# Performance work log

Hardware: AMD Instinct MI355X
Metric: run time of the kernel (lower is better)

## Reference

```python
import jax, jax.numpy as jnp
import numpy as np

B, S, D = 4, 4096, 128

def setup_inputs() -> dict:
    key = jax.random.key(0)
    kq, kk, kv = jax.random.split(key, 3)
    q = jax.random.normal(kq, (B, S, D), dtype=jnp.float32)
    k = jax.random.normal(kk, (B, S, D), dtype=jnp.float32)
    v = jax.random.normal(kv, (B, S, D), dtype=jnp.float32)
    return {"q": q, "k": k, "v": v}

def reference(q, k, v):
    d_model = q.shape[-1]
    scale = 1.0 / jnp.sqrt(jnp.asarray(d_model, q.dtype))
    # [B, S, S] scores
    scores = jnp.einsum('bqd,bkd->bqk', q, k) * scale
    s = q.shape[1]
    causal = jnp.tril(jnp.ones((s, s), dtype=bool))
    neg_inf = jnp.asarray(-jnp.inf, scores.dtype)
    scores = jnp.where(causal[None, :, :], scores, neg_inf)
    attn = jax.nn.softmax(scores, axis=-1)
    return jnp.einsum('bqk,bkd->bqd', attn, v)
```

## Files before the change

### kernel.cpp

```cpp
#include <hip/hip_runtime.h>


#define B_   4
#define S_   4096
#define D_   128
#define BM   64
#define BN   64
#define NT_  (S_ / BM)
#define RMAX 4
#define PSTR 72
#define BLOB_SHORTS 16384

typedef __attribute__((ext_vector_type(8))) short bf16x8;
typedef __attribute__((ext_vector_type(4))) float f32x4;

__device__ __forceinline__ short f2bf(float x) {
    unsigned u = __builtin_bit_cast(unsigned, x);
    unsigned r = (u + 0x7fffu + ((u >> 16) & 1u)) >> 16;
    return (short)r;
}
__device__ __forceinline__ float ex2(float x) { return __builtin_amdgcn_exp2f(x); }

__device__ __forceinline__ void gl_lds16(const short* g, short* l) {
    __builtin_amdgcn_global_load_lds(
        (const __attribute__((address_space(1))) unsigned int*)g,
        (__attribute__((address_space(3))) unsigned int*)l, 16, 0, 0);
}

__global__ __launch_bounds__(256) void prep(const float* __restrict__ Qg,
                                            const float* __restrict__ Kg,
                                            const float* __restrict__ Vg,
                                            short* __restrict__ Qbf,
                                            short* __restrict__ KV)
{
    __shared__ short vt[64][136];

    const int x = blockIdx.x;
    const int b = x & 3, tile = x >> 2;
    const int tid = threadIdx.x;
    const int n = tid >> 2, q = tid & 3;
    const size_t rowbase = ((size_t)b * S_ + (size_t)tile * 64 + n) * D_ + q * 32;
    short* blob = KV + (size_t)(b * NT_ + tile) * BLOB_SHORTS;

    const float SC = 0.12751740f;
    {
        const float4* src = reinterpret_cast<const float4*>(Qg + rowbase);
        short* dst = Qbf + rowbase;
#pragma unroll
        for (int j = 0; j < 4; ++j) {
            float4 a = src[2 * j], c = src[2 * j + 1];
            bf16x8 v;
            v[0] = f2bf(a.x * SC); v[1] = f2bf(a.y * SC); v[2] = f2bf(a.z * SC); v[3] = f2bf(a.w * SC);
            v[4] = f2bf(c.x * SC); v[5] = f2bf(c.y * SC); v[6] = f2bf(c.z * SC); v[7] = f2bf(c.w * SC);
            *reinterpret_cast<bf16x8*>(dst + j * 8) = v;
        }
    }
    {
        const float4* src = reinterpret_cast<const float4*>(Kg + rowbase);
#pragma unroll
        for (int j = 0; j < 4; ++j) {
            float4 a = src[2 * j], c = src[2 * j + 1];
            bf16x8 v;
            v[0] = f2bf(a.x); v[1] = f2bf(a.y); v[2] = f2bf(a.z); v[3] = f2bf(a.w);
            v[4] = f2bf(c.x); v[5] = f2bf(c.y); v[6] = f2bf(c.z); v[7] = f2bf(c.w);
            const int G = q * 4 + j;
            const int p = (G & 8) | ((G & 7) ^ (n & 7));
            *reinterpret_cast<bf16x8*>(blob + n * 128 + p * 8) = v;
        }
    }
    {
        const float4* src = reinterpret_cast<const float4*>(Vg + rowbase);
#pragma unroll
        for (int j = 0; j < 4; ++j) {
            float4 a = src[2 * j], c = src[2 * j + 1];
            bf16x8 v;
            v[0] = f2bf(a.x); v[1] = f2bf(a.y); v[2] = f2bf(a.z); v[3] = f2bf(a.w);
            v[4] = f2bf(c.x); v[5] = f2bf(c.y); v[6] = f2bf(c.z); v[7] = f2bf(c.w);
            *reinterpret_cast<bf16x8*>(&vt[n][q * 32 + j * 8]) = v;
        }
    }
    __syncthreads();
    {
        const int d = tid >> 1, jj = tid & 1;
#pragma unroll
        for (int j = 0; j < 4; ++j) {
            const int G = jj * 4 + j;
            bf16x8 g;
#pragma unroll
            for (int i = 0; i < 8; ++i) g[i] = vt[G * 8 + i][d];
            const int p = G ^ (d & 7);
            *reinterpret_cast<bf16x8*>(blob + 8192 + d * 64 + p * 8) = g;
        }
    }
}

template<bool SPLIT>
__global__ __launch_bounds__(256) void fa_fwd(const short* __restrict__ Qbf,
                                              const short* __restrict__ KV,
                                              float* __restrict__ Og,
                                              float* __restrict__ Op,
                                              float* __restrict__ Ml,
                                              int R)
{
    __shared__ short lkv[2][BLOB_SHORTS];
    __shared__ short lp[4 * 16 * PSTR];

    const int tid  = threadIdx.x;
    const int wv   = tid >> 6;
    const int lane = tid & 63;
    const int m    = lane & 15;
    const int quad = lane >> 4;
    const int m7   = m & 7;

    int batch, t, lo, hi, chunk_id;
    {
        const int id = blockIdx.x;
        batch = id & 3;
        if (SPLIT) {
            int u = id >> 2;
            int tt = u / R;
            int r  = u - tt * R;
            t  = NT_ - 1 - tt;
            lo = r * (t + 1) / R;
            hi = (r + 1) * (t + 1) / R;
            chunk_id = (batch * NT_ + t) * R + r;
            if (lo >= hi) return;
        } else {
            t  = NT_ - 1 - (id >> 2);
            lo = 0; hi = t + 1; chunk_id = 0;
        }
    }

    bf16x8 qf[4];
    {
        const short* qp = Qbf + ((size_t)batch * S_ + (size_t)t * BM + wv * 16 + m) * D_ + quad * 8;
#pragma unroll
        for (int c = 0; c < 4; ++c)
            qf[c] = *reinterpret_cast<const bf16x8*>(qp + c * 32);
    }

    f32x4 acc[8];
#pragma unroll
    for (int i = 0; i < 8; ++i) acc[i] = (f32x4){0.f, 0.f, 0.f, 0.f};
    float mrun[4], lrun[4];
#pragma unroll
    for (int r = 0; r < 4; ++r) { mrun[r] = -__builtin_inff(); lrun[r] = 0.f; }

    short* pw = lp + wv * 16 * PSTR;

    const size_t tilebase = (size_t)batch * NT_ * BLOB_SHORTS;
#define STAGE(KT, BUF) do {                                                   \
        const short* g_ = KV + tilebase + (size_t)(KT) * BLOB_SHORTS          \
                          + wv * 4096 + lane * 8;                             \
        short* l_ = (BUF) + wv * 4096;                                        \
        _Pragma("unroll")                                                     \
        for (int c_ = 0; c_ < 8; ++c_)                                        \
            gl_lds16(g_ + c_ * 512, l_ + c_ * 512);                           \
    } while (0)

    STAGE(lo, lkv[0]);

    for (int kt = lo; kt < hi; ++kt) {
        short* cur = lkv[(kt - lo) & 1];
        short* nxt = lkv[(kt - lo + 1) & 1];
        __syncthreads();
        if (kt + 1 < hi) STAGE(kt + 1, nxt);

        const short* lk = cur;
        const short* lv = cur + 8192;

        f32x4 s[4];
#pragma unroll
        for (int nt = 0; nt < 4; ++nt) s[nt] = (f32x4){0.f, 0.f, 0.f, 0.f};
#pragma unroll
        for (int c = 0; c < 4; ++c) {
            const int p = ((c >> 1) * 8) | ((((c & 1) * 4) | quad) ^ m7);
#pragma unroll
            for (int nt = 0; nt < 4; ++nt) {
                bf16x8 kf = *reinterpret_cast<const bf16x8*>(lk + nt * 2048 + m * 128 + p * 8);
                s[nt] = __builtin_amdgcn_mfma_f32_16x16x32_bf16(qf[c], kf, s[nt], 0, 0, 0);
            }
        }

        if (kt == t) {
            const int qloc = wv * 16 + quad * 4;
#pragma unroll
            for (int nt = 0; nt < 4; ++nt) {
                const int kloc = nt * 16 + m;
#pragma unroll
                for (int r = 0; r < 4; ++r)
                    if (kloc > qloc + r) s[nt][r] = -__builtin_inff();
            }
        }

#pragma unroll
        for (int r = 0; r < 4; ++r) {
            float mx = fmaxf(fmaxf(s[0][r], s[1][r]), fmaxf(s[2][r], s[3][r]));
#pragma unroll
            for (int off = 1; off < 16; off <<= 1) mx = fmaxf(mx, __shfl_xor(mx, off));
            float mnew = fmaxf(mrun[r], mx);
            float al   = ex2(mrun[r] - mnew);
            mrun[r] = mnew;
            float p0 = ex2(s[0][r] - mnew);
            float p1 = ex2(s[1][r] - mnew);
            float p2 = ex2(s[2][r] - mnew);
            float p3 = ex2(s[3][r] - mnew);
            s[0][r] = p0; s[1][r] = p1; s[2][r] = p2; s[3][r] = p3;
            float sum = (p0 + p1) + (p2 + p3);
#pragma unroll
            for (int off = 1; off < 16; off <<= 1) sum += __shfl_xor(sum, off);
            lrun[r] = lrun[r] * al + sum;
#pragma unroll
            for (int ct = 0; ct < 8; ++ct) acc[ct][r] *= al;
        }

#pragma unroll
        for (int nt = 0; nt < 4; ++nt)
#pragma unroll
            for (int r = 0; r < 4; ++r)
                pw[(quad * 4 + r) * PSTR + nt * 16 + m] = f2bf(s[nt][r]);

#pragma unroll
        for (int ks = 0; ks < 2; ++ks) {
            bf16x8 pf = *reinterpret_cast<const bf16x8*>(pw + m * PSTR + ks * 32 + quad * 8);
            const int p = (ks * 4 + quad) ^ m7;
#pragma unroll
            for (int ct = 0; ct < 8; ++ct) {
                bf16x8 vf = *reinterpret_cast<const bf16x8*>(lv + ct * 1024 + m * 64 + p * 8);
                acc[ct] = __builtin_amdgcn_mfma_f32_16x16x32_bf16(pf, vf, acc[ct], 0, 0, 0);
            }
        }
    }
#undef STAGE

    const int row0 = wv * 16 + quad * 4;
    if (SPLIT) {
        float* ob = Op + (size_t)chunk_id * (BM * D_);
#pragma unroll
        for (int r = 0; r < 4; ++r)
#pragma unroll
            for (int ct = 0; ct < 8; ++ct)
                ob[(row0 + r) * D_ + ct * 16 + m] = acc[ct][r];
        if (m == 0) {
            float* mlb = Ml + (size_t)chunk_id * (BM * 2);
#pragma unroll
            for (int r = 0; r < 4; ++r) {
                mlb[(row0 + r) * 2]     = mrun[r];
                mlb[(row0 + r) * 2 + 1] = lrun[r];
            }
        }
    } else {
        const size_t obase = ((size_t)batch * S_ + (size_t)t * BM + row0) * D_;
#pragma unroll
        for (int r = 0; r < 4; ++r) {
            float inv = 1.0f / lrun[r];
#pragma unroll
            for (int ct = 0; ct < 8; ++ct)
                Og[obase + (size_t)r * D_ + ct * 16 + m] = acc[ct][r] * inv;
        }
    }
}

template<int RR>
__global__ __launch_bounds__(256) void fa_merge(const float* __restrict__ Op,
                                                const float* __restrict__ Ml,
                                                float* __restrict__ Og)
{
    const int x   = blockIdx.x;
    const int btq = x >> 2;
    const int seg = x & 3;
    const int t   = btq & (NT_ - 1);
    const int row = seg * 16 + (threadIdx.x >> 4);
    const int cg  = threadIdx.x & 15;
    const size_t cbase = (size_t)btq * RR;

    float mg = -__builtin_inff();
#pragma unroll
    for (int r = 0; r < RR; ++r) {
        int lo = r * (t + 1) / RR, hi = (r + 1) * (t + 1) / RR;
        if (lo < hi) mg = fmaxf(mg, Ml[(cbase + r) * (BM * 2) + row * 2]);
    }
    float l = 0.f;
    f32x4 a0 = (f32x4){0.f, 0.f, 0.f, 0.f}, a1 = a0;
#pragma unroll
    for (int r = 0; r < RR; ++r) {
        int lo = r * (t + 1) / RR, hi = (r + 1) * (t + 1) / RR;
        if (lo >= hi) continue;
        float mr = Ml[(cbase + r) * (BM * 2) + row * 2];
        float lr = Ml[(cbase + r) * (BM * 2) + row * 2 + 1];
        float w  = ex2(mr - mg);
        l += lr * w;
        const f32x4* op = reinterpret_cast<const f32x4*>(Op + (cbase + r) * (BM * D_) + row * D_ + cg * 8);
        a0 += w * op[0]; a1 += w * op[1];
    }
    float inv = 1.0f / l;
    f32x4* og = reinterpret_cast<f32x4*>(Og + (size_t)btq * (BM * D_) + row * D_ + cg * 8);
    og[0] = a0 * inv; og[1] = a1 * inv;
}

extern "C" void kernel_launch(void* const* d_in, const int* in_sizes, int n_in,
                              void* d_out, int out_size, void* d_ws, size_t ws_size,
                              hipStream_t stream) {
    const float* q = (const float*)d_in[0];
    const float* k = (const float*)d_in[1];
    const float* v = (const float*)d_in[2];
    float* o = (float*)d_out;

    const size_t QBF_BYTES = (size_t)B_ * S_ * D_ * 2;
    const size_t KV_BYTES  = (size_t)B_ * NT_ * BLOB_SHORTS * 2;
    const size_t PREFIX    = QBF_BYTES + KV_BYTES;
    const size_t O_FLOATS  = (size_t)B_ * NT_ * BM * D_;
    const size_t ML_FLOATS = (size_t)B_ * NT_ * BM * 2;
    const size_t PER_R     = (O_FLOATS + ML_FLOATS) * sizeof(float);

    char* ws = (char*)d_ws;
    short* Qbf = (short*)ws;
    short* KV  = (short*)(ws + QBF_BYTES);

    int R = 0;
    if (ws_size > PREFIX) {
        R = (int)((ws_size - PREFIX) / PER_R);
        if (R > RMAX) R = RMAX;
    }

    prep<<<dim3(B_ * NT_), 256, 0, stream>>>(q, k, v, Qbf, KV);

    if (R >= 1) {
        float* Op = (float*)(ws + PREFIX);
        float* Ml = Op + (size_t)R * O_FLOATS;
        fa_fwd<true><<<dim3(B_ * NT_ * R), 256, 0, stream>>>(Qbf, KV, nullptr, Op, Ml, R);
        switch (R) {
            case 1: fa_merge<1><<<dim3(B_ * NT_ * 4), 256, 0, stream>>>(Op, Ml, o); break;
            case 2: fa_merge<2><<<dim3(B_ * NT_ * 4), 256, 0, stream>>>(Op, Ml, o); break;
            case 3: fa_merge<3><<<dim3(B_ * NT_ * 4), 256, 0, stream>>>(Op, Ml, o); break;
            default: fa_merge<4><<<dim3(B_ * NT_ * 4), 256, 0, stream>>>(Op, Ml, o); break;
        }
    } else {
        fa_fwd<false><<<dim3(B_ * NT_), 256, 0, stream>>>(Qbf, KV, o, nullptr, nullptr, 1);
    }
}
```

Before: 134.9 us.

## Transpose QK MFMA, shuffle P in registers, single LDS buffer, finer prep/merge grids

New measurement: 195.4 us. +44.9%, slower.

```diff
diff --git a/kernel.cpp b/kernel.cpp
--- a/kernel.cpp
+++ b/kernel.cpp
@@ -8,7 +8,6 @@
 #define BN   64
 #define NT_  (S_ / BM)
 #define RMAX 4
-#define PSTR 72
 #define BLOB_SHORTS 16384
 
 typedef __attribute__((ext_vector_type(8))) short bf16x8;
@@ -20,11 +19,8 @@
     return (short)r;
 }
 __device__ __forceinline__ float ex2(float x) { return __builtin_amdgcn_exp2f(x); }
-
-__device__ __forceinline__ void gl_lds16(const short* g, short* l) {
-    __builtin_amdgcn_global_load_lds(
-        (const __attribute__((address_space(1))) unsigned int*)g,
-        (__attribute__((address_space(3))) unsigned int*)l, 16, 0, 0);
+__device__ __forceinline__ unsigned pkbf(float lo, float hi) {
+    return (unsigned)(unsigned short)f2bf(lo) | ((unsigned)(unsigned short)f2bf(hi) << 16);
 }
 
 __global__ __launch_bounds__(256) void prep(const float* __restrict__ Qg,
@@ -33,61 +29,55 @@
                                             short* __restrict__ Qbf,
                                             short* __restrict__ KV)
 {
-    __shared__ short vt[64][136];
-
-    const int x = blockIdx.x;
-    const int b = x & 3, tile = x >> 2;
+    __shared__ short vt[64][40];
+    const int id  = blockIdx.x;
     const int tid = threadIdx.x;
-    const int n = tid >> 2, q = tid & 3;
-    const size_t rowbase = ((size_t)b * S_ + (size_t)tile * 64 + n) * D_ + q * 32;
-    short* blob = KV + (size_t)(b * NT_ + tile) * BLOB_SHORTS;
-
     const float SC = 0.12751740f;
-    {
-        const float4* src = reinterpret_cast<const float4*>(Qg + rowbase);
-        short* dst = Qbf + rowbase;
-#pragma unroll
-        for (int j = 0; j < 4; ++j) {
-            float4 a = src[2 * j], c = src[2 * j + 1];
+
+    if (id < 1024) {
+        const int b = id & 3, tile = (id >> 2) & 63, q4 = id >> 8;
+        const int n = q4 * 16 + (tid >> 4);
+        const int G = tid & 15;
+        const size_t rowoff = ((size_t)b * S_ + (size_t)tile * 64 + n) * D_ + G * 8;
+        short* blob = KV + (size_t)(b * NT_ + tile) * BLOB_SHORTS;
+        {
+            float4 a = *reinterpret_cast<const float4*>(Qg + rowoff);
+            float4 c = *reinterpret_cast<const float4*>(Qg + rowoff + 4);
             bf16x8 v;
             v[0] = f2bf(a.x * SC); v[1] = f2bf(a.y * SC); v[2] = f2bf(a.z * SC); v[3] = f2bf(a.w * SC);
             v[4] = f2bf(c.x * SC); v[5] = f2bf(c.y * SC); v[6] = f2bf(c.z * SC); v[7] = f2bf(c.w * SC);
-            *reinterpret_cast<bf16x8*>(dst + j * 8) = v;
-        }
-    }
-    {
-        const float4* src = reinterpret_cast<const float4*>(Kg + rowbase);
-#pragma unroll
-        for (int j = 0; j < 4; ++j) {
-            float4 a = src[2 * j], c = src[2 * j + 1];
+            *reinterpret_cast<bf16x8*>(Qbf + rowoff) = v;
+        }
+        {
+            float4 a = *reinterpret_cast<const float4*>(Kg + rowoff);
+            float4 c = *reinterpret_cast<const float4*>(Kg + rowoff + 4);
             bf16x8 v;
             v[0] = f2bf(a.x); v[1] = f2bf(a.y); v[2] = f2bf(a.z); v[3] = f2bf(a.w);
             v[4] = f2bf(c.x); v[5] = f2bf(c.y); v[6] = f2bf(c.z); v[7] = f2bf(c.w);
-            const int G = q * 4 + j;
             const int p = (G & 8) | ((G & 7) ^ (n & 7));
             *reinterpret_cast<bf16x8*>(blob + n * 128 + p * 8) = v;
         }
-    }
-    {
-        const float4* src = reinterpret_cast<const float4*>(Vg + rowbase);
-#pragma unroll
-        for (int j = 0; j < 4; ++j) {
-            float4 a = src[2 * j], c = src[2 * j + 1];
+    } else {
+        const int u = id - 1024;
+        const int b = u & 3, tile = (u >> 2) & 63, dq = u >> 8;
+        short* blob = KV + (size_t)(b * NT_ + tile) * BLOB_SHORTS;
+        {
+            const int n = tid >> 2, c8 = tid & 3;
+            const size_t off = ((size_t)b * S_ + (size_t)tile * 64 + n) * D_ + dq * 32 + c8 * 8;
+            float4 a = *reinterpret_cast<const float4*>(Vg + off);
+            float4 c = *reinterpret_cast<const float4*>(Vg + off + 4);
             bf16x8 v;
             v[0] = f2bf(a.x); v[1] = f2bf(a.y); v[2] = f2bf(a.z); v[3] = f2bf(a.w);
             v[4] = f2bf(c.x); v[5] = f2bf(c.y); v[6] = f2bf(c.z); v[7] = f2bf(c.w);
-            *reinterpret_cast<bf16x8*>(&vt[n][q * 32 + j * 8]) = v;
-        }
-    }
-    __syncthreads();
-    {
-        const int d = tid >> 1, jj = tid & 1;
-#pragma unroll
-        for (int j = 0; j < 4; ++j) {
-            const int G = jj * 4 + j;
+            *reinterpret_cast<bf16x8*>(&vt[n][c8 * 8]) = v;
+        }
+        __syncthreads();
+        {
+            const int dl = tid >> 3, G = tid & 7;
+            const int d  = dq * 32 + dl;
             bf16x8 g;
 #pragma unroll
-            for (int i = 0; i < 8; ++i) g[i] = vt[G * 8 + i][d];
+            for (int i = 0; i < 8; ++i) g[i] = vt[G * 8 + i][dl];
             const int p = G ^ (d & 7);
             *reinterpret_cast<bf16x8*>(blob + 8192 + d * 64 + p * 8) = g;
         }
@@ -95,15 +85,14 @@
 }
 
 template<bool SPLIT>
-__global__ __launch_bounds__(256) void fa_fwd(const short* __restrict__ Qbf,
-                                              const short* __restrict__ KV,
-                                              float* __restrict__ Og,
-                                              float* __restrict__ Op,
-                                              float* __restrict__ Ml,
-                                              int R)
+__global__ __launch_bounds__(256, 4) void fa_fwd(const short* __restrict__ Qbf,
+                                                 const short* __restrict__ KV,
+                                                 float* __restrict__ Og,
+                                                 float* __restrict__ Op,
+                                                 float* __restrict__ Ml,
+                                                 int R)
 {
-    __shared__ short lkv[2][BLOB_SHORTS];
-    __shared__ short lp[4 * 16 * PSTR];
+    __shared__ short lkv[BLOB_SHORTS];
 
     const int tid  = threadIdx.x;
     const int wv   = tid >> 6;
@@ -142,87 +131,110 @@
     f32x4 acc[8];
 #pragma unroll
     for (int i = 0; i < 8; ++i) acc[i] = (f32x4){0.f, 0.f, 0.f, 0.f};
-    float mrun[4], lrun[4];
-#pragma unroll
-    for (int r = 0; r < 4; ++r) { mrun[r] = -__builtin_inff(); lrun[r] = 0.f; }
-
-    short* pw = lp + wv * 16 * PSTR;
+    float mrun = -__builtin_inff(), lrun = 0.f;
 
     const size_t tilebase = (size_t)batch * NT_ * BLOB_SHORTS;
-#define STAGE(KT, BUF) do {                                                   \
-        const short* g_ = KV + tilebase + (size_t)(KT) * BLOB_SHORTS          \
-                          + wv * 4096 + lane * 8;                             \
-        short* l_ = (BUF) + wv * 4096;                                        \
+    int4 pfr[8];
+#define LOADR(KT) do {                                                        \
+        const short* g_ = KV + tilebase + (size_t)(KT) * BLOB_SHORTS + tid * 8;\
         _Pragma("unroll")                                                     \
         for (int c_ = 0; c_ < 8; ++c_)                                        \
-            gl_lds16(g_ + c_ * 512, l_ + c_ * 512);                           \
+            pfr[c_] = *reinterpret_cast<const int4*>(g_ + c_ * 2048);         \
     } while (0)
 
-    STAGE(lo, lkv[0]);
+    LOADR(lo);
 
     for (int kt = lo; kt < hi; ++kt) {
-        short* cur = lkv[(kt - lo) & 1];
-        short* nxt = lkv[(kt - lo + 1) & 1];
         __syncthreads();
-        if (kt + 1 < hi) STAGE(kt + 1, nxt);
-
-        const short* lk = cur;
-        const short* lv = cur + 8192;
-
-        f32x4 s[4];
-#pragma unroll
-        for (int nt = 0; nt < 4; ++nt) s[nt] = (f32x4){0.f, 0.f, 0.f, 0.f};
+        {
+            short* l_ = lkv + tid * 8;
+#pragma unroll
+            for (int c_ = 0; c_ < 8; ++c_)
+                *reinterpret_cast<int4*>(l_ + c_ * 2048) = pfr[c_];
+        }
+        __syncthreads();
+        if (kt + 1 < hi) LOADR(kt + 1);
+
+        const short* lk = lkv;
+        const short* lv = lkv + 8192;
+
+        f32x4 st[4];
+#pragma unroll
+        for (int nt = 0; nt < 4; ++nt) st[nt] = (f32x4){0.f, 0.f, 0.f, 0.f};
 #pragma unroll
         for (int c = 0; c < 4; ++c) {
             const int p = ((c >> 1) * 8) | ((((c & 1) * 4) | quad) ^ m7);
 #pragma unroll
             for (int nt = 0; nt < 4; ++nt) {
                 bf16x8 kf = *reinterpret_cast<const bf16x8*>(lk + nt * 2048 + m * 128 + p * 8);
-                s[nt] = __builtin_amdgcn_mfma_f32_16x16x32_bf16(qf[c], kf, s[nt], 0, 0, 0);
+                st[nt] = __builtin_amdgcn_mfma_f32_16x16x32_bf16(kf, qf[c], st[nt], 0, 0, 0);
             }
         }
 
         if (kt == t) {
-            const int qloc = wv * 16 + quad * 4;
-#pragma unroll
-            for (int nt = 0; nt < 4; ++nt) {
-                const int kloc = nt * 16 + m;
+            const int qloc = wv * 16 + m;
+#pragma unroll
+            for (int nt = 0; nt < 4; ++nt)
 #pragma unroll
                 for (int r = 0; r < 4; ++r)
-                    if (kloc > qloc + r) s[nt][r] = -__builtin_inff();
+                    if (nt * 16 + quad * 4 + r > qloc) st[nt][r] = -__builtin_inff();
+        }
+
+        float mx = -__builtin_inff();
+#pragma unroll
+        for (int nt = 0; nt < 4; ++nt)
+#pragma unroll
+            for (int r = 0; r < 4; ++r) mx = fmaxf(mx, st[nt][r]);
+        mx = fmaxf(mx, __shfl_xor(mx, 16));
+        mx = fmaxf(mx, __shfl_xor(mx, 32));
+        const float mnew = fmaxf(mrun, mx);
+        const float al   = ex2(mrun - mnew);
+        mrun = mnew;
+        float sum = 0.f;
+#pragma unroll
+        for (int nt = 0; nt < 4; ++nt)
+#pragma unroll
+            for (int r = 0; r < 4; ++r) {
+                float pv = ex2(st[nt][r] - mnew);
+                st[nt][r] = pv;
+                sum += pv;
             }
-        }
-
+        sum += __shfl_xor(sum, 16);
+        sum += __shfl_xor(sum, 32);
+        lrun = lrun * al + sum;
 #pragma unroll
         for (int r = 0; r < 4; ++r) {
-            float mx = fmaxf(fmaxf(s[0][r], s[1][r]), fmaxf(s[2][r], s[3][r]));
-#pragma unroll
-            for (int off = 1; off < 16; off <<= 1) mx = fmaxf(mx, __shfl_xor(mx, off));
-            float mnew = fmaxf(mrun[r], mx);
-            float al   = ex2(mrun[r] - mnew);
-            mrun[r] = mnew;
-            float p0 = ex2(s[0][r] - mnew);
-            float p1 = ex2(s[1][r] - mnew);
-            float p2 = ex2(s[2][r] - mnew);
-            float p3 = ex2(s[3][r] - mnew);
-            s[0][r] = p0; s[1][r] = p1; s[2][r] = p2; s[3][r] = p3;
-            float sum = (p0 + p1) + (p2 + p3);
-#pragma unroll
-            for (int off = 1; off < 16; off <<= 1) sum += __shfl_xor(sum, off);
-            lrun[r] = lrun[r] * al + sum;
-#pragma unroll
-            for (int ct = 0; ct < 8; ++ct) acc[ct][r] *= al;
-        }
-
-#pragma unroll
-        for (int nt = 0; nt < 4; ++nt)
-#pragma unroll
-            for (int r = 0; r < 4; ++r)
-                pw[(quad * 4 + r) * PSTR + nt * 16 + m] = f2bf(s[nt][r]);
+            float alq = __shfl(al, quad * 4 + r);
+#pragma unroll
+            for (int ct = 0; ct < 8; ++ct) acc[ct][r] *= alq;
+        }
+
+        unsigned pk[8];
+#pragma unroll
+        for (int nt = 0; nt < 4; ++nt) {
+            pk[nt * 2]     = pkbf(st[nt][0], st[nt][1]);
+            pk[nt * 2 + 1] = pkbf(st[nt][2], st[nt][3]);
+        }
+        const int srcA = ((quad & 1) << 5) + m;
+        const int srcB = srcA + 16;
+        const bool loq = quad < 2;
 
 #pragma unroll
         for (int ks = 0; ks < 2; ++ks) {
-            bf16x8 pf = *reinterpret_cast<const bf16x8*>(pw + m * PSTR + ks * 32 + quad * 8);
+            unsigned w0a = __shfl((int)pk[4 * ks + 0], srcA);
+            unsigned w0b = __shfl((int)pk[4 * ks + 2], srcA);
+            unsigned w1a = __shfl((int)pk[4 * ks + 1], srcA);
+            unsigned w1b = __shfl((int)pk[4 * ks + 3], srcA);
+            unsigned w2a = __shfl((int)pk[4 * ks + 0], srcB);
+            unsigned w2b = __shfl((int)pk[4 * ks + 2], srcB);
+            unsigned w3a = __shfl((int)pk[4 * ks + 1], srcB);
+            unsigned w3b = __shfl((int)pk[4 * ks + 3], srcB);
+            int4 wi;
+            wi.x = (int)(loq ? w0a : w0b);
+            wi.y = (int)(loq ? w1a : w1b);
+            wi.z = (int)(loq ? w2a : w2b);
+            wi.w = (int)(loq ? w3a : w3b);
+            bf16x8 pf = __builtin_bit_cast(bf16x8, wi);
             const int p = (ks * 4 + quad) ^ m7;
 #pragma unroll
             for (int ct = 0; ct < 8; ++ct) {
@@ -231,7 +243,7 @@
             }
         }
     }
-#undef STAGE
+#undef LOADR
 
     const int row0 = wv * 16 + quad * 4;
     if (SPLIT) {
@@ -241,22 +253,20 @@
 #pragma unroll
             for (int ct = 0; ct < 8; ++ct)
                 ob[(row0 + r) * D_ + ct * 16 + m] = acc[ct][r];
-        if (m == 0) {
-            float* mlb = Ml + (size_t)chunk_id * (BM * 2);
-#pragma unroll
-            for (int r = 0; r < 4; ++r) {
-                mlb[(row0 + r) * 2]     = mrun[r];
-                mlb[(row0 + r) * 2 + 1] = lrun[r];
-            }
+        if (lane < 16) {
+            float* mlb = Ml + (size_t)chunk_id * (BM * 2) + (wv * 16 + lane) * 2;
+            mlb[0] = mrun;
+            mlb[1] = lrun;
         }
     } else {
+        const float inv = 1.0f / lrun;
         const size_t obase = ((size_t)batch * S_ + (size_t)t * BM + row0) * D_;
 #pragma unroll
         for (int r = 0; r < 4; ++r) {
-            float inv = 1.0f / lrun[r];
+            float invq = __shfl(inv, quad * 4 + r);
 #pragma unroll
             for (int ct = 0; ct < 8; ++ct)
-                Og[obase + (size_t)r * D_ + ct * 16 + m] = acc[ct][r] * inv;
+                Og[obase + (size_t)r * D_ + ct * 16 + m] = acc[ct][r] * invq;
         }
     }
 }
@@ -267,11 +277,11 @@
                                                 float* __restrict__ Og)
 {
     const int x   = blockIdx.x;
-    const int btq = x >> 2;
-    const int seg = x & 3;
+    const int btq = x >> 3;
+    const int oct = x & 7;
     const int t   = btq & (NT_ - 1);
-    const int row = seg * 16 + (threadIdx.x >> 4);
-    const int cg  = threadIdx.x & 15;
+    const int row = oct * 8 + (threadIdx.x >> 5);
+    const int cg  = threadIdx.x & 31;
     const size_t cbase = (size_t)btq * RR;
 
     float mg = -__builtin_inff();
@@ -281,7 +291,7 @@
         if (lo < hi) mg = fmaxf(mg, Ml[(cbase + r) * (BM * 2) + row * 2]);
     }
     float l = 0.f;
-    f32x4 a0 = (f32x4){0.f, 0.f, 0.f, 0.f}, a1 = a0;
+    f32x4 a = (f32x4){0.f, 0.f, 0.f, 0.f};
 #pragma unroll
     for (int r = 0; r < RR; ++r) {
         int lo = r * (t + 1) / RR, hi = (r + 1) * (t + 1) / RR;
@@ -290,12 +300,9 @@
         float lr = Ml[(cbase + r) * (BM * 2) + row * 2 + 1];
         float w  = ex2(mr - mg);
         l += lr * w;
-        const f32x4* op = reinterpret_cast<const f32x4*>(Op + (cbase + r) * (BM * D_) + row * D_ + cg * 8);
-        a0 += w * op[0]; a1 += w * op[1];
-    }
-    float inv = 1.0f / l;
-    f32x4* og = reinterpret_cast<f32x4*>(Og + (size_t)btq * (BM * D_) + row * D_ + cg * 8);
-    og[0] = a0 * inv; og[1] = a1 * inv;
+        a += w * *reinterpret_cast<const f32x4*>(Op + (cbase + r) * (BM * D_) + row * D_ + cg * 4);
+    }
+    *reinterpret_cast<f32x4*>(Og + (size_t)btq * (BM * D_) + row * D_ + cg * 4) = a * (1.0f / l);
 }
 
 extern "C" void kernel_launch(void* const* d_in, const int* in_sizes, int n_in,
@@ -323,17 +330,17 @@
         if (R > RMAX) R = RMAX;
     }
 
-    prep<<<dim3(B_ * NT_), 256, 0, stream>>>(q, k, v, Qbf, KV);
+    prep<<<dim3(2048), 256, 0, stream>>>(q, k, v, Qbf, KV);
 
     if (R >= 1) {
         float* Op = (float*)(ws + PREFIX);
         float* Ml = Op + (size_t)R * O_FLOATS;
         fa_fwd<true><<<dim3(B_ * NT_ * R), 256, 0, stream>>>(Qbf, KV, nullptr, Op, Ml, R);
         switch (R) {
-            case 1: fa_merge<1><<<dim3(B_ * NT_ * 4), 256, 0, stream>>>(Op, Ml, o); break;
-            case 2: fa_merge<2><<<dim3(B_ * NT_ * 4), 256, 0, stream>>>(Op, Ml, o); break;
-            case 3: fa_merge<3><<<dim3(B_ * NT_ * 4), 256, 0, stream>>>(Op, Ml, o); break;
-            default: fa_merge<4><<<dim3(B_ * NT_ * 4), 256, 0, stream>>>(Op, Ml, o); break;
+            case 1: fa_merge<1><<<dim3(B_ * NT_ * 8), 256, 0, stream>>>(Op, Ml, o); break;
+            case 2: fa_merge<2><<<dim3(B_ * NT_ * 8), 256, 0, stream>>>(Op, Ml, o); break;
+            case 3: fa_merge<3><<<dim3(B_ * NT_ * 8), 256, 0, stream>>>(Op, Ml, o); break;
+            default: fa_merge<4><<<dim3(B_ * NT_ * 8), 256, 0, stream>>>(Op, Ml, o); break;
         }
     } else {
         fa_fwd<false><<<dim3(B_ * NT_), 256, 0, stream>>>(Qbf, KV, o, nullptr, nullptr, 1);
```
